# Performance work log

Measured on AMD Instinct MI355X. Metric: run time of the kernel, lower is better.

Reference implementation:

```python
import jax, jax.numpy as jnp
import numpy as np

B, S, E = 2, 2048, 4096
H, KVH, D = 32, 8, 128
GROUPS = H // KVH
MAX_POS = 4096
ROPE_THETA = 10000.0


def _rope_tables(max_pos, dim, theta):
    inv_freq = 1.0 / (theta ** (jnp.arange(0, dim, 2, dtype=jnp.float32) / dim))
    t = jnp.arange(max_pos, dtype=jnp.float32)
    freqs = jnp.einsum('i,j->ij', t, inv_freq)        # [max_pos, dim/2]
    emb = jnp.concatenate([freqs, freqs], axis=-1)    # [max_pos, dim]
    return jnp.cos(emb), jnp.sin(emb)


def _rotate_half(x):
    x1, x2 = x[..., : x.shape[-1] // 2], x[..., x.shape[-1] // 2:]
    return jnp.concatenate([-x2, x1], axis=-1)


def setup_inputs() -> dict:
    key = jax.random.key(0)
    ks = jax.random.split(key, 8)
    scale_w = 1.0 / np.sqrt(E)
    query = jax.random.normal(ks[0], (B, S, E), dtype=jnp.float32)
    k_in = jax.random.normal(ks[1], (B, S, E), dtype=jnp.float32)
    v_in = jax.random.normal(ks[2], (B, S, E), dtype=jnp.float32)
    position_ids = jnp.broadcast_to(jnp.arange(S, dtype=jnp.int64), (B, S))
    # causal mask: 1 where attending allowed, 0 elsewhere
    src_mask = jnp.tril(jnp.ones((S, S), dtype=jnp.int32))
    src_mask = jnp.broadcast_to(src_mask, (B, S, S))
    Wq = jax.random.normal(ks[3], (E, H * D), dtype=jnp.float32) * scale_w
    Wk = jax.random.normal(ks[4], (E, KVH * D), dtype=jnp.float32) * scale_w
    Wv = jax.random.normal(ks[5], (E, KVH * D), dtype=jnp.float32) * scale_w
    Wo = jax.random.normal(ks[6], (H * D, E), dtype=jnp.float32) * scale_w
    return {"query": query, "key": k_in, "value": v_in,
            "position_ids": position_ids, "src_mask": src_mask,
            "Wq": Wq, "Wk": Wk, "Wv": Wv, "Wo": Wo}


def reference(query, key, value, position_ids, src_mask, Wq, Wk, Wv, Wo):
    nb, q_len, _ = query.shape
    # projections -> [B, heads, S, D]
    q = (query @ Wq).reshape(nb, q_len, H, D).transpose(0, 2, 1, 3)
    k = (key @ Wk).reshape(nb, q_len, KVH, D).transpose(0, 2, 1, 3)
    v = (value @ Wv).reshape(nb, q_len, KVH, D).transpose(0, 2, 1, 3)
    # RoPE
    cos_t, sin_t = _rope_tables(MAX_POS, D, ROPE_THETA)
    cos = cos_t[position_ids][:, None]  # [B,1,S,D]
    sin = sin_t[position_ids][:, None]
    q = q * cos + _rotate_half(q) * sin
    k = k * cos + _rotate_half(k) * sin
    # repeat_kv (interleave groups) -> [B,H,S,D]
    k = jnp.repeat(k, GROUPS, axis=1)
    v = jnp.repeat(v, GROUPS, axis=1)
    # attention core
    scores = jnp.einsum('bhqd,bhkd->bhqk', q, k) / jnp.sqrt(jnp.float32(D))
    mask = src_mask[:, None]  # [B,1,S,S]
    scores = jnp.where(mask == 0, jnp.float32(-1e9), scores)
    attn = jax.nn.softmax(scores, axis=-1)
    x = jnp.einsum('bhqk,bhkd->bhqd', attn, v)
    x = x.transpose(0, 2, 1, 3).reshape(nb, q_len, H * D)
    return x @ Wo
```

## Files before the change

### kernel.cpp

```cpp
#include <hip/hip_runtime.h>
#include <stdint.h>

#define B_ 2
#define S_ 2048
#define E_ 4096
#define H_ 32
#define KVH_ 8
#define D_ 128

typedef __bf16 bf16_t;
typedef __bf16 bf16x8 __attribute__((ext_vector_type(8)));
typedef __bf16 bf16x4 __attribute__((ext_vector_type(4)));
typedef float f32x4 __attribute__((ext_vector_type(4)));

__device__ __forceinline__ void gl2lds16(const void* g, void* l) {
  __builtin_amdgcn_global_load_lds(
      (__attribute__((address_space(1))) void*)(uintptr_t)g,
      (__attribute__((address_space(3))) void*)(uint32_t)(uintptr_t)l,
      16, 0, 0);
}

__global__ void cvt_f32_bf16(const float* __restrict__ in, bf16_t* __restrict__ out, int n4) {
  int i = blockIdx.x * 256 + threadIdx.x;
  if (i < n4) {
    float4 v = ((const float4*)in)[i];
    bf16x4 o;
    o.x = (bf16_t)v.x; o.y = (bf16_t)v.y; o.z = (bf16_t)v.z; o.w = (bf16_t)v.w;
    ((bf16x4*)out)[i] = o;
  }
}

__global__ void transpose_cvt(const float* __restrict__ in, bf16_t* __restrict__ out,
                              int R, int C) {
  __shared__ float t[32][33];
  int r0 = blockIdx.y * 32, c0 = blockIdx.x * 32;
  int tx = threadIdx.x & 31, tg = threadIdx.x >> 5;
#pragma unroll
  for (int k = 0; k < 4; ++k) {
    int r = tg * 4 + k;
    t[r][tx] = in[(long)(r0 + r) * C + c0 + tx];
  }
  __syncthreads();
#pragma unroll
  for (int k = 0; k < 4; ++k) {
    int r = tg * 4 + k;
    out[(long)(c0 + r) * R + r0 + tx] = (bf16_t)t[tx][r];
  }
}

__global__ void transpose_v(const float* __restrict__ Vtmp, bf16_t* __restrict__ Vt) {
  __shared__ float t[32][33];
  int z = blockIdx.z, b = z >> 3, kv = z & 7;
  const float* in = Vtmp + (long)b * S_ * (KVH_ * D_) + kv * D_;
  bf16_t* out = Vt + ((long)(b * KVH_ + kv)) * D_ * S_;
  int s0 = blockIdx.y * 32, d0 = blockIdx.x * 32;
  int tx = threadIdx.x & 31, tg = threadIdx.x >> 5;
#pragma unroll
  for (int k = 0; k < 4; ++k) {
    int r = tg * 4 + k;
    t[r][tx] = in[(long)(s0 + r) * (KVH_ * D_) + d0 + tx];
  }
  __syncthreads();
#pragma unroll
  for (int k = 0; k < 4; ++k) {
    int r = tg * 4 + k;
    out[(long)(d0 + r) * S_ + s0 + tx] = (bf16_t)t[tx][r];
  }
}

__global__ void rope_cvt(const float* __restrict__ T, bf16_t* __restrict__ out,
                         const int* __restrict__ pos, int NH, float scale) {
  long idx = (long)blockIdx.x * 256 + threadIdx.x;
  int j = (int)(idx & 63);
  long t = idx >> 6;
  int s = (int)(t % S_); t /= S_;
  int nh = (int)(t % NH);
  int b = (int)(t / NH);
  long row = ((long)b * S_ + s) * ((long)NH * D_) + (long)nh * D_;
  float x1 = T[row + j];
  float x2 = T[row + j + 64];
  float p = (float)pos[(long)b * S_ + s];
  float inv = expf(-(float)j * (9.210340371976184f / 64.0f));
  float fr = p * inv;
  float c = cosf(fr), sn = sinf(fr);
  long ob = (((long)b * NH + nh) * S_ + s) * D_;
  out[ob + j]      = (bf16_t)((x1 * c - x2 * sn) * scale);
  out[ob + j + 64] = (bf16_t)((x2 * c + x1 * sn) * scale);
}

__global__ __launch_bounds__(256, 2) void gemm_bt(
    const bf16_t* __restrict__ A, const bf16_t* __restrict__ Bt,
    float* __restrict__ C, int M, int N, int K) {
  __shared__ bf16_t As[128 * 64];
  __shared__ bf16_t Bs[128 * 64];
  const int tid = threadIdx.x;
  const int lane = tid & 63;
  const int wave = tid >> 6;
  const int m0 = blockIdx.y * 128, n0 = blockIdx.x * 128;
  const int wm = (wave >> 1) * 64, wn = (wave & 1) * 64;
  const int ln = lane & 15, quad = lane >> 4;
  const int srow = lane >> 3;
  const int sg = lane & 7;

  f32x4 acc[4][4] = {};

  for (int kb = 0; kb < K; kb += 64) {
    __syncthreads();
#pragma unroll
    for (int it = 0; it < 4; ++it) {
      int c = wave * 4 + it;
      int row = c * 8 + srow;
      int g = sg ^ (row & 7);
      gl2lds16(A + (long)(m0 + row) * K + kb + g * 8, &As[c * 512 + lane * 8]);
      gl2lds16(Bt + (long)(n0 + row) * K + kb + g * 8, &Bs[c * 512 + lane * 8]);
    }
    __syncthreads();
#pragma unroll
    for (int ks = 0; ks < 2; ++ks) {
      bf16x8 af[4], bfr[4];
      const int go = ((ks * 4 + quad) ^ (ln & 7)) * 8;
#pragma unroll
      for (int i = 0; i < 4; ++i)
        af[i] = *(const bf16x8*)&As[(wm + i * 16 + ln) * 64 + go];
#pragma unroll
      for (int j = 0; j < 4; ++j)
        bfr[j] = *(const bf16x8*)&Bs[(wn + j * 16 + ln) * 64 + go];
#pragma unroll
      for (int i = 0; i < 4; ++i)
#pragma unroll
        for (int j = 0; j < 4; ++j)
          acc[i][j] = __builtin_amdgcn_mfma_f32_16x16x32_bf16(af[i], bfr[j], acc[i][j], 0, 0, 0);
    }
  }
#pragma unroll
  for (int i = 0; i < 4; ++i)
#pragma unroll
    for (int j = 0; j < 4; ++j)
#pragma unroll
      for (int r = 0; r < 4; ++r) {
        int m = m0 + wm + i * 16 + quad * 4 + r;
        int n = n0 + wn + j * 16 + ln;
        C[(long)m * N + n] = acc[i][j][r];
      }
}

__global__ __launch_bounds__(256, 1) void flash_attn(
    const bf16_t* __restrict__ Q, const bf16_t* __restrict__ Kr,
    const bf16_t* __restrict__ Vt, bf16_t* __restrict__ X) {
  __shared__ bf16_t Ks[128 * 128];
  __shared__ bf16_t Vs[128 * 128];
  const int tid = threadIdx.x, lane = tid & 63, wave = tid >> 6;
  const int ln = lane & 15, quad = lane >> 4;
  const int qi = (int)(gridDim.x - 1 - blockIdx.x);
  const int h = blockIdx.y, b = blockIdx.z;
  const int kv = h >> 2;
  const bf16_t* Kbase = Kr + (((long)b * KVH_ + kv) * S_) * D_;
  const bf16_t* Vbase = Vt + (((long)b * KVH_ + kv) * D_) * S_;
  bf16_t* Pw = &Ks[wave * 4096];

  bf16x8 aq[2][4];
  {
    const bf16_t* Qw = Q + (((long)b * H_ + h) * S_ + qi * 128 + wave * 32) * D_;
#pragma unroll
    for (int i = 0; i < 2; ++i)
#pragma unroll
      for (int ks = 0; ks < 4; ++ks)
        aq[i][ks] = *(const bf16x8*)(Qw + (i * 16 + ln) * D_ + ks * 32 + quad * 8);
  }

  f32x4 o_acc[2][8] = {};
  float m_cur[2][4], l_cur[2][4];
#pragma unroll
  for (int i = 0; i < 2; ++i)
#pragma unroll
    for (int r = 0; r < 4; ++r) { m_cur[i][r] = -__builtin_inff(); l_cur[i][r] = 0.f; }

  for (int jt = 0; jt <= qi; ++jt) {
    __syncthreads();
    const bf16_t* Kt = Kbase + (long)jt * 128 * D_;
#pragma unroll
    for (int it = 0; it < 8; ++it) {
      int c = wave * 8 + it;
      int row = c * 4 + quad;
      int g = ln ^ (row & 15);
      gl2lds16(Kt + (long)row * D_ + g * 8, &Ks[c * 512 + lane * 8]);
      gl2lds16(Vbase + (long)row * S_ + jt * 128 + g * 8, &Vs[c * 512 + lane * 8]);
    }
    __syncthreads();

    f32x4 s_acc[2][8] = {};
#pragma unroll
    for (int ks = 0; ks < 4; ++ks) {
      bf16x8 bk[8];
      const int go = ((ks * 4 + quad) ^ ln) * 8;
#pragma unroll
      for (int j = 0; j < 8; ++j)
        bk[j] = *(const bf16x8*)&Ks[(j * 16 + ln) * 128 + go];
#pragma unroll
      for (int i = 0; i < 2; ++i)
#pragma unroll
        for (int j = 0; j < 8; ++j)
          s_acc[i][j] = __builtin_amdgcn_mfma_f32_16x16x32_bf16(aq[i][ks], bk[j], s_acc[i][j], 0, 0, 0);
    }
    __syncthreads();

#pragma unroll
    for (int i = 0; i < 2; ++i) {
      float rmax[4];
#pragma unroll
      for (int r = 0; r < 4; ++r) rmax[r] = -__builtin_inff();
#pragma unroll
      for (int j = 0; j < 8; ++j)
#pragma unroll
        for (int r = 0; r < 4; ++r) {
          float v = s_acc[i][j][r];
          if (jt == qi) {
            int qrow = wave * 32 + i * 16 + quad * 4 + r;
            int kcol = j * 16 + ln;
            if (kcol > qrow) v = -__builtin_inff();
          }
          s_acc[i][j][r] = v;
          rmax[r] = fmaxf(rmax[r], v);
        }
#pragma unroll
      for (int r = 0; r < 4; ++r) {
        float v = rmax[r];
        v = fmaxf(v, __shfl_xor(v, 1));
        v = fmaxf(v, __shfl_xor(v, 2));
        v = fmaxf(v, __shfl_xor(v, 4));
        v = fmaxf(v, __shfl_xor(v, 8));
        rmax[r] = v;
      }
      float alpha[4];
#pragma unroll
      for (int r = 0; r < 4; ++r) {
        float mn = fmaxf(m_cur[i][r], rmax[r]);
        alpha[r] = exp2f(m_cur[i][r] - mn);
        m_cur[i][r] = mn;
      }
      float rsum[4] = {0.f, 0.f, 0.f, 0.f};
#pragma unroll
      for (int j = 0; j < 8; ++j)
#pragma unroll
        for (int r = 0; r < 4; ++r) {
          float p = exp2f(s_acc[i][j][r] - m_cur[i][r]);
          s_acc[i][j][r] = p;
          rsum[r] += p;
        }
#pragma unroll
      for (int r = 0; r < 4; ++r) {
        float v = rsum[r];
        v += __shfl_xor(v, 1);
        v += __shfl_xor(v, 2);
        v += __shfl_xor(v, 4);
        v += __shfl_xor(v, 8);
        l_cur[i][r] = l_cur[i][r] * alpha[r] + v;
      }
#pragma unroll
      for (int j = 0; j < 8; ++j)
#pragma unroll
        for (int r = 0; r < 4; ++r)
          o_acc[i][j][r] *= alpha[r];
#pragma unroll
      for (int j = 0; j < 8; ++j)
#pragma unroll
        for (int r = 0; r < 4; ++r) {
          int prow = i * 16 + quad * 4 + r;
          int pg = (j * 2 + (ln >> 3)) ^ (prow & 15);
          Pw[prow * 128 + pg * 8 + (ln & 7)] = (bf16_t)s_acc[i][j][r];
        }
    }

#pragma unroll
    for (int ks = 0; ks < 4; ++ks) {
      bf16x8 ap[2], bv[8];
      const int go = ((ks * 4 + quad) ^ ln) * 8;
#pragma unroll
      for (int i = 0; i < 2; ++i)
        ap[i] = *(const bf16x8*)&Pw[(i * 16 + ln) * 128 + go];
#pragma unroll
      for (int j = 0; j < 8; ++j)
        bv[j] = *(const bf16x8*)&Vs[(j * 16 + ln) * 128 + go];
#pragma unroll
      for (int i = 0; i < 2; ++i)
#pragma unroll
        for (int j = 0; j < 8; ++j)
          o_acc[i][j] = __builtin_amdgcn_mfma_f32_16x16x32_bf16(ap[i], bv[j], o_acc[i][j], 0, 0, 0);
    }
  }

#pragma unroll
  for (int i = 0; i < 2; ++i) {
    float rl[4];
#pragma unroll
    for (int r = 0; r < 4; ++r) rl[r] = 1.0f / l_cur[i][r];
#pragma unroll
    for (int j = 0; j < 8; ++j)
#pragma unroll
      for (int r = 0; r < 4; ++r) {
        int q = qi * 128 + wave * 32 + i * 16 + quad * 4 + r;
        int dcol = j * 16 + ln;
        float o = o_acc[i][j][r] * rl[r];
        X[((long)b * S_ + q) * (H_ * D_) + (long)h * D_ + dcol] = (bf16_t)o;
      }
  }
}

extern "C" void kernel_launch(void* const* d_in, const int* in_sizes, int n_in,
                              void* d_out, int out_size, void* d_ws, size_t ws_size,
                              hipStream_t stream) {
  const float* query = (const float*)d_in[0];
  const float* key   = (const float*)d_in[1];
  const float* value = (const float*)d_in[2];
  const int*   pos   = (const int*)d_in[3];
  const float* Wq = (const float*)d_in[5];
  const float* Wk = (const float*)d_in[6];
  const float* Wv = (const float*)d_in[7];
  const float* Wo = (const float*)d_in[8];
  float* out = (float*)d_out;

  char* ws = (char*)d_ws;
  size_t off = 0;
  auto alloc = [&](size_t bytes) {
    char* p = ws + off;
    off += (bytes + 1023) & ~(size_t)1023;
    return p;
  };
  bf16_t* Wqt = (bf16_t*)alloc(33554432);
  bf16_t* Wkt = (bf16_t*)alloc(8388608);
  bf16_t* Wvt = (bf16_t*)alloc(8388608);
  bf16_t* Wot = (bf16_t*)alloc(33554432);
  bf16_t* Xq  = (bf16_t*)alloc(33554432);
  bf16_t* Xk  = (bf16_t*)alloc(33554432);
  bf16_t* Xv  = (bf16_t*)alloc(33554432);
  float*  Ktmp = (float*)alloc(16777216);
  float*  Vtmp = (float*)alloc(16777216);
  float*  Qtmp = out;
  bf16_t* Qr = Xk;
  bf16_t* Kr = Xv;
  bf16_t* Vt = (bf16_t*)((char*)Xv + 8388608);
  bf16_t* X  = Xq;

  const int n4 = B_ * S_ * E_ / 4;
  cvt_f32_bf16<<<n4 / 256, 256, 0, stream>>>(query, Xq, n4);
  cvt_f32_bf16<<<n4 / 256, 256, 0, stream>>>(key, Xk, n4);
  cvt_f32_bf16<<<n4 / 256, 256, 0, stream>>>(value, Xv, n4);

  transpose_cvt<<<dim3(128, 128), 256, 0, stream>>>(Wq, Wqt, 4096, 4096);
  transpose_cvt<<<dim3(32, 128), 256, 0, stream>>>(Wk, Wkt, 4096, 1024);
  transpose_cvt<<<dim3(32, 128), 256, 0, stream>>>(Wv, Wvt, 4096, 1024);
  transpose_cvt<<<dim3(128, 128), 256, 0, stream>>>(Wo, Wot, 4096, 4096);

  gemm_bt<<<dim3(32, 32), 256, 0, stream>>>(Xq, Wqt, Qtmp, 4096, 4096, 4096);
  gemm_bt<<<dim3(8, 32), 256, 0, stream>>>(Xk, Wkt, Ktmp, 4096, 1024, 4096);
  gemm_bt<<<dim3(8, 32), 256, 0, stream>>>(Xv, Wvt, Vtmp, 4096, 1024, 4096);

  rope_cvt<<<(B_ * H_ * S_ * 64) / 256, 256, 0, stream>>>(Qtmp, Qr, pos, H_, 0.12751743f);
  rope_cvt<<<(B_ * KVH_ * S_ * 64) / 256, 256, 0, stream>>>(Ktmp, Kr, pos, KVH_, 1.0f);
  transpose_v<<<dim3(4, 64, 16), 256, 0, stream>>>(Vtmp, Vt);

  flash_attn<<<dim3(16, 32, 2), 256, 0, stream>>>(Qr, Kr, Vt, X);

  gemm_bt<<<dim3(32, 32), 256, 0, stream>>>(X, Wot, out, 4096, 4096, 4096);
}
```

Measured before the change: 1.271 ms.

## Load K/V fragments directly from global memory and remap attention grid for XCD locality

The flash attention kernel stops staging K and V tiles through shared memory with block-wide barriers. Each wave now reads its MFMA operands straight from global memory, and only the P tile stays in LDS. The launch becomes a 1D grid whose block index is permuted so that blocks sharing a KV head and batch land on the same XCD's L2, and MFMA sections get raised wave priority. This removes barrier stalls and LDS traffic, but the four waves now each fetch the same K/V data separately and depend on L2 hits, and the direct loads are less coalesced (16-byte pieces at a stride of a full row).

```diff
diff --git a/kernel.cpp b/kernel.cpp
--- a/kernel.cpp
+++ b/kernel.cpp
@@ -147,16 +147,19 @@
 __global__ __launch_bounds__(256, 1) void flash_attn(
     const bf16_t* __restrict__ Q, const bf16_t* __restrict__ Kr,
     const bf16_t* __restrict__ Vt, bf16_t* __restrict__ X) {
-  __shared__ bf16_t Ks[128 * 128];
-  __shared__ bf16_t Vs[128 * 128];
+  __shared__ bf16_t Plds[4 * 32 * 128];
   const int tid = threadIdx.x, lane = tid & 63, wave = tid >> 6;
   const int ln = lane & 15, quad = lane >> 4;
-  const int qi = (int)(gridDim.x - 1 - blockIdx.x);
-  const int h = blockIdx.y, b = blockIdx.z;
+
+  const int d = blockIdx.x;
+  const int wid = (d & 7) * 128 + (d >> 3);
+  const int qi = 15 - (wid & 15);
+  const int h = (wid >> 4) & 31;
+  const int b = wid >> 9;
   const int kv = h >> 2;
   const bf16_t* Kbase = Kr + (((long)b * KVH_ + kv) * S_) * D_;
   const bf16_t* Vbase = Vt + (((long)b * KVH_ + kv) * D_) * S_;
-  bf16_t* Pw = &Ks[wave * 4096];
+  bf16_t* Pw = &Plds[wave * 4096];
 
   bf16x8 aq[2][4];
   {
@@ -176,33 +179,23 @@
     for (int r = 0; r < 4; ++r) { m_cur[i][r] = -__builtin_inff(); l_cur[i][r] = 0.f; }
 
   for (int jt = 0; jt <= qi; ++jt) {
-    __syncthreads();
     const bf16_t* Kt = Kbase + (long)jt * 128 * D_;
-#pragma unroll
-    for (int it = 0; it < 8; ++it) {
-      int c = wave * 8 + it;
-      int row = c * 4 + quad;
-      int g = ln ^ (row & 15);
-      gl2lds16(Kt + (long)row * D_ + g * 8, &Ks[c * 512 + lane * 8]);
-      gl2lds16(Vbase + (long)row * S_ + jt * 128 + g * 8, &Vs[c * 512 + lane * 8]);
-    }
-    __syncthreads();
 
     f32x4 s_acc[2][8] = {};
 #pragma unroll
     for (int ks = 0; ks < 4; ++ks) {
       bf16x8 bk[8];
-      const int go = ((ks * 4 + quad) ^ ln) * 8;
-#pragma unroll
-      for (int j = 0; j < 8; ++j)
-        bk[j] = *(const bf16x8*)&Ks[(j * 16 + ln) * 128 + go];
+#pragma unroll
+      for (int j = 0; j < 8; ++j)
+        bk[j] = *(const bf16x8*)(Kt + (long)(j * 16 + ln) * D_ + ks * 32 + quad * 8);
+      __builtin_amdgcn_s_setprio(1);
 #pragma unroll
       for (int i = 0; i < 2; ++i)
 #pragma unroll
         for (int j = 0; j < 8; ++j)
           s_acc[i][j] = __builtin_amdgcn_mfma_f32_16x16x32_bf16(aq[i][ks], bk[j], s_acc[i][j], 0, 0, 0);
-    }
-    __syncthreads();
+      __builtin_amdgcn_s_setprio(0);
+    }
 
 #pragma unroll
     for (int i = 0; i < 2; ++i) {
@@ -280,12 +273,14 @@
         ap[i] = *(const bf16x8*)&Pw[(i * 16 + ln) * 128 + go];
 #pragma unroll
       for (int j = 0; j < 8; ++j)
-        bv[j] = *(const bf16x8*)&Vs[(j * 16 + ln) * 128 + go];
+        bv[j] = *(const bf16x8*)(Vbase + (long)(j * 16 + ln) * S_ + jt * 128 + ks * 32 + quad * 8);
+      __builtin_amdgcn_s_setprio(1);
 #pragma unroll
       for (int i = 0; i < 2; ++i)
 #pragma unroll
         for (int j = 0; j < 8; ++j)
           o_acc[i][j] = __builtin_amdgcn_mfma_f32_16x16x32_bf16(ap[i], bv[j], o_acc[i][j], 0, 0, 0);
+      __builtin_amdgcn_s_setprio(0);
     }
   }
 
@@ -359,7 +354,7 @@
   rope_cvt<<<(B_ * KVH_ * S_ * 64) / 256, 256, 0, stream>>>(Ktmp, Kr, pos, KVH_, 1.0f);
   transpose_v<<<dim3(4, 64, 16), 256, 0, stream>>>(Vtmp, Vt);
 
-  flash_attn<<<dim3(16, 32, 2), 256, 0, stream>>>(Qr, Kr, Vt, X);
+  flash_attn<<<dim3(1024), 256, 0, stream>>>(Qr, Kr, Vt, X);
 
   gemm_bt<<<dim3(32, 32), 256, 0, stream>>>(X, Wot, out, 4096, 4096, 4096);
 }
```

Measured after the change: 1.252 ms. No clear change (-1.5%).
